# Optimization experiments

Hardware: AMD Instinct MI355X
Metric: run time of the kernel (lower is better)

Reference implementation:

```python
import jax, jax.numpy as jnp
import numpy as np

N_NODES = 100000
N_EDGES = 3200000
D_IN = 256
D_HID = 256
D_OUT = 64


def setup_inputs() -> dict:
    key = jax.random.key(0)
    k1, k2, k3, k4 = jax.random.split(key, 4)
    x = jax.random.normal(k1, (N_NODES, D_IN), dtype=jnp.float32)
    edge_index = jax.random.randint(k2, (2, N_EDGES), 0, N_NODES, dtype=jnp.int32)
    W1 = jax.random.normal(k3, (D_IN, D_HID), dtype=jnp.float32) / np.sqrt(D_IN)
    b1 = jnp.zeros((D_HID,), dtype=jnp.float32)
    W2 = jax.random.normal(k4, (D_HID, D_OUT), dtype=jnp.float32) / np.sqrt(D_HID)
    b2 = jnp.zeros((D_OUT,), dtype=jnp.float32)
    return {"x": x, "edge_index": edge_index, "W1": W1, "b1": b1, "W2": W2, "b2": b2}


def _gcn_conv(x, src, dst, norm, W, b, n_nodes):
    # dense linear transform, then normalized scatter-add aggregation
    h = x @ W  # [N, out]
    msg = norm[:, None] * h[src]  # gather + scale, [E+N, out]
    out = jax.ops.segment_sum(msg, dst, num_segments=n_nodes)
    return out + b


def reference(x, edge_index, W1, b1, W2, b2):
    n = x.shape[0]
    # add self-loops (PyG GCNConv default)
    loops = jnp.arange(n, dtype=edge_index.dtype)
    src = jnp.concatenate([edge_index[0], loops])
    dst = jnp.concatenate([edge_index[1], loops])
    # symmetric normalization deg^{-1/2}[src] * deg^{-1/2}[dst]
    deg = jax.ops.segment_sum(jnp.ones_like(src, dtype=x.dtype), dst, num_segments=n)
    dinv = jnp.where(deg > 0, jax.lax.rsqrt(jnp.maximum(deg, 1.0)), 0.0)
    norm = dinv[src] * dinv[dst]

    h = _gcn_conv(x, src, dst, norm, W1, b1, n)
    h = jax.nn.relu(h)
    # dropout is identity at inference
    h = _gcn_conv(h, src, dst, norm, W2, b2, n)
    return jax.nn.log_softmax(h, axis=1)
```

## Files before the change

kernel.cpp:

```cpp
#include <hip/hip_runtime.h>
#include <hip/hip_bf16.h>


typedef __bf16 bf16;
typedef bf16 bf16x8 __attribute__((ext_vector_type(8)));
typedef float f32x4 __attribute__((ext_vector_type(4)));
typedef float f32x2 __attribute__((ext_vector_type(2)));

#define NBLK 256

__global__ __launch_bounds__(256) void k_b1(const int* __restrict__ edge, int E, int chunk,
                                            int NB, int* __restrict__ gcnt) {
    __shared__ int cnt[512];
    int tid = threadIdx.x;
    for (int i = tid; i < NB; i += 256) cnt[i] = 0;
    __syncthreads();
    int s = blockIdx.x * chunk, e = min(s + chunk, E);
    for (int i = s + tid; i < e; i += 256) atomicAdd(&cnt[edge[E + i] >> 9], 1);
    __syncthreads();
    for (int i = tid; i < NB; i += 256) gcnt[blockIdx.x * NB + i] = cnt[i];
}

__global__ void k_b2(const int* __restrict__ gcnt, int NB, int E, int* __restrict__ bstart) {
    __shared__ int col[256];
    int k = threadIdx.x;
    int sum = 0;
    if (k < NB)
        for (int b = 0; b < NBLK; ++b) sum += gcnt[b * NB + k];
    col[k] = sum;
    __syncthreads();
    for (int o = 1; o < 256; o <<= 1) {
        int v = (k >= o) ? col[k - o] : 0;
        __syncthreads();
        col[k] += v;
        __syncthreads();
    }
    if (k < NB) bstart[k] = col[k] - sum;
    if (k == 0) bstart[NB] = E;
}

__global__ void k_b2b(int* __restrict__ gcnt, int NB, const int* __restrict__ bstart) {
    __shared__ int col[256];
    int b = threadIdx.x;
    int k = blockIdx.x;
    int v = gcnt[b * NB + k];
    col[b] = v;
    __syncthreads();
    for (int o = 1; o < 256; o <<= 1) {
        int t = (b >= o) ? col[b - o] : 0;
        __syncthreads();
        col[b] += t;
        __syncthreads();
    }
    gcnt[b * NB + k] = bstart[k] + col[b] - v;
}

__global__ __launch_bounds__(256) void k_b3(const int* __restrict__ edge, int E, int chunk,
                                            int NB, const int* __restrict__ base,
                                            int* __restrict__ ebuf) {
    __shared__ int cnt[512];
    __shared__ int bs[512];
    int tid = threadIdx.x;
    for (int i = tid; i < NB; i += 256) {
        cnt[i] = 0;
        bs[i] = base[blockIdx.x * NB + i];
    }
    __syncthreads();
    int s = blockIdx.x * chunk, e = min(s + chunk, E);
    for (int i = s + tid; i < e; i += 256) {
        int sv = edge[i], dv = edge[E + i];
        int k = dv >> 9;
        int r = atomicAdd(&cnt[k], 1);
        ebuf[bs[k] + r] = sv | ((dv & 511) << 17);
    }
}

__global__ __launch_bounds__(256) void k_b45(const int* __restrict__ ebuf,
                                             const int* __restrict__ bstart,
                                             const float* __restrict__ scale, int n, int E,
                                             int NB, int* __restrict__ off,
                                             float* __restrict__ dinv,
                                             float* __restrict__ ws) {
    __shared__ int cnt[512];
    __shared__ int red[256];
    int tid = threadIdx.x;
    int k = blockIdx.x;
    cnt[tid] = 0;
    cnt[tid + 256] = 0;
    __syncthreads();
    int s = bstart[k], e = bstart[k + 1];
    for (int i = s + tid; i < e; i += 256) atomicAdd(&cnt[(ebuf[i] >> 17) & 511], 1);
    __syncthreads();
    int c0 = cnt[tid * 2], c1 = cnt[tid * 2 + 1];
    int sum = c0 + c1;
    red[tid] = sum;
    __syncthreads();
    for (int o = 1; o < 256; o <<= 1) {
        int v = (tid >= o) ? red[tid - o] : 0;
        __syncthreads();
        red[tid] += v;
        __syncthreads();
    }
    int ex = red[tid] - sum;
    int base = k << 9;
    int g0 = base + tid * 2, g1 = g0 + 1;
    int o0 = s + ex, o1 = s + ex + c0;
    if (g0 < n) {
        off[g0] = o0;
        float d0 = rsqrtf((float)(c0 + 1));
        dinv[g0] = d0;
        ws[g0] = d0 * scale[g0];
    } else if (g0 == n) off[g0] = o0;
    if (g1 < n) {
        off[g1] = o1;
        float d1 = rsqrtf((float)(c1 + 1));
        dinv[g1] = d1;
        ws[g1] = d1 * scale[g1];
    } else if (g1 == n) off[g1] = o1;
    if (k == NB - 1 && tid == 0) off[n] = E;
}

__global__ __launch_bounds__(256) void k_b6(const int* __restrict__ ebuf,
                                            const int* __restrict__ bstart,
                                            const int* __restrict__ off,
                                            const float* __restrict__ ws, int n,
                                            int2* __restrict__ pair) {
    __shared__ int cnt[512];
    __shared__ int offl[512];
    int tid = threadIdx.x;
    int k = blockIdx.x;
    int base = k << 9;
    cnt[tid] = 0;
    cnt[tid + 256] = 0;
    offl[tid] = (base + tid < n) ? off[base + tid] : 0;
    offl[tid + 256] = (base + 256 + tid < n) ? off[base + 256 + tid] : 0;
    __syncthreads();
    int s = bstart[k], e = bstart[k + 1];
    for (int i = s + tid; i < e; i += 256) {
        int pk = ebuf[i];
        int sv = pk & 0x1ffff;
        int node = (pk >> 17) & 511;
        int r = atomicAdd(&cnt[node], 1);
        pair[offl[node] + r] = make_int2(sv << 8, __float_as_int(ws[sv]));
    }
}

__global__ __launch_bounds__(256) void k_quant(const float* __restrict__ x,
                                               unsigned char* __restrict__ xq,
                                               float* __restrict__ scale, int n) {
    int row = blockIdx.x * 4 + (threadIdx.x >> 6);
    int lane = threadIdx.x & 63;
    if (row >= n) return;
    f32x4 v = ((const f32x4*)x)[(size_t)row * 64 + lane];
    float m = fmaxf(fmaxf(fabsf(v[0]), fabsf(v[1])), fmaxf(fabsf(v[2]), fabsf(v[3])));
    for (int o = 32; o > 0; o >>= 1) m = fmaxf(m, __shfl_xor(m, o));
    m = fmaxf(m, 1e-20f);
    float inv = 127.0f / m;
    int b0 = (__float2int_rn(v[0] * inv) + 128) & 255;
    int b1 = (__float2int_rn(v[1] * inv) + 128) & 255;
    int b2 = (__float2int_rn(v[2] * inv) + 128) & 255;
    int b3 = (__float2int_rn(v[3] * inv) + 128) & 255;
    ((int*)xq)[(size_t)row * 64 + lane] = b0 | (b1 << 8) | (b2 << 16) | (b3 << 24);
    if (lane == 0) scale[row] = m / 127.0f;
}

__global__ __launch_bounds__(256) void k_quant2(const bf16* __restrict__ tb,
                                                const float* __restrict__ dinv,
                                                unsigned char* __restrict__ tq,
                                                float* __restrict__ w2v, int n) {
    int t = blockIdx.x * 256 + threadIdx.x;
    int row = t >> 3;
    int l8 = t & 7;
    if (row >= n) return;
    bf16x8 v = ((const bf16x8*)tb)[(size_t)row * 8 + l8];
    float f[8], m = 0.0f;
#pragma unroll
    for (int j = 0; j < 8; ++j) { f[j] = (float)v[j]; m = fmaxf(m, fabsf(f[j])); }
    for (int o = 4; o > 0; o >>= 1) m = fmaxf(m, __shfl_xor(m, o));
    m = fmaxf(m, 1e-20f);
    float inv = 127.0f / m;
    int lo = 0, hi = 0;
#pragma unroll
    for (int j = 0; j < 4; ++j) lo |= ((__float2int_rn(f[j] * inv) + 128) & 255) << (8 * j);
#pragma unroll
    for (int j = 0; j < 4; ++j) hi |= ((__float2int_rn(f[4 + j] * inv) + 128) & 255) << (8 * j);
    ((int2*)tq)[(size_t)row * 8 + l8] = make_int2(lo, hi);
    if (l8 == 0) w2v[row] = dinv[row] * (m / 127.0f);
}

__global__ void k_wt(const float* __restrict__ W1, const float* __restrict__ W2,
                     bf16* __restrict__ W1t, bf16* __restrict__ W2t) {
    int b = blockIdx.x;
    int k = threadIdx.x;
    if (b < 256) W1t[b * 256 + k] = (bf16)W1[k * 256 + b];
    else { int nc = b - 256; W2t[nc * 256 + k] = (bf16)W2[k * 64 + nc]; }
}

__device__ __forceinline__ void acc16(f32x2 a[8], uint4 t, float w, float& wsum) {
    wsum += w;
    f32x2 w2 = {w, w};
    unsigned u0 = t.x, u1 = t.y, u2 = t.z, u3 = t.w;
    f32x2 c;
    c[0] = (float)(u0 & 255u);         c[1] = (float)((u0 >> 8) & 255u);  a[0] += w2 * c;
    c[0] = (float)((u0 >> 16) & 255u); c[1] = (float)(u0 >> 24);         a[1] += w2 * c;
    c[0] = (float)(u1 & 255u);         c[1] = (float)((u1 >> 8) & 255u);  a[2] += w2 * c;
    c[0] = (float)((u1 >> 16) & 255u); c[1] = (float)(u1 >> 24);         a[3] += w2 * c;
    c[0] = (float)(u2 & 255u);         c[1] = (float)((u2 >> 8) & 255u);  a[4] += w2 * c;
    c[0] = (float)((u2 >> 16) & 255u); c[1] = (float)(u2 >> 24);         a[5] += w2 * c;
    c[0] = (float)(u3 & 255u);         c[1] = (float)((u3 >> 8) & 255u);  a[6] += w2 * c;
    c[0] = (float)((u3 >> 16) & 255u); c[1] = (float)(u3 >> 24);         a[7] += w2 * c;
}

__device__ __forceinline__ void acc8(f32x2 a[4], int2 t, float w, float& wsum) {
    wsum += w;
    f32x2 w2 = {w, w};
    unsigned u0 = (unsigned)t.x, u1 = (unsigned)t.y;
    f32x2 c;
    c[0] = (float)(u0 & 255u);         c[1] = (float)((u0 >> 8) & 255u);  a[0] += w2 * c;
    c[0] = (float)((u0 >> 16) & 255u); c[1] = (float)(u0 >> 24);         a[1] += w2 * c;
    c[0] = (float)(u1 & 255u);         c[1] = (float)((u1 >> 8) & 255u);  a[2] += w2 * c;
    c[0] = (float)((u1 >> 16) & 255u); c[1] = (float)(u1 >> 24);         a[3] += w2 * c;
}

__global__ __launch_bounds__(256) void k_agg1(const unsigned char* __restrict__ xq,
                                              const float* __restrict__ wsv,
                                              const int* __restrict__ off,
                                              const int2* __restrict__ pair,
                                              const float* __restrict__ dinv,
                                              bf16* __restrict__ ax, int n) {
    int wv = blockIdx.x * 4 + (threadIdx.x >> 6);
    int lane = threadIdx.x & 63;
    int node = wv * 4 + (lane >> 4);
    int l16 = lane & 15;
    if (node >= n) return;
    int s0 = off[node], s1 = off[node + 1];
    float dv = dinv[node];
    const unsigned char* xqb = xq + l16 * 16;
    f32x2 a[8] = {};
    float wsum = 0.0f;
    uint4 xs = *(const uint4*)(xqb + (size_t)node * 256);
    acc16(a, xs, wsv[node], wsum);
    int e = s0;
    if (s1 - s0 >= 8) {
        int2 p[8];
#pragma unroll
        for (int q = 0; q < 8; ++q) p[q] = pair[s0 + q];
        e = s0 + 8;
        for (; e + 8 <= s1; e += 8) {
            uint4 t[8];
#pragma unroll
            for (int q = 0; q < 8; ++q)
                t[q] = *(const uint4*)(xqb + (unsigned)p[q].x);
            int2 pn[8];
#pragma unroll
            for (int q = 0; q < 8; ++q) pn[q] = pair[e + q];
#pragma unroll
            for (int q = 0; q < 8; ++q) acc16(a, t[q], __int_as_float(p[q].y), wsum);
#pragma unroll
            for (int q = 0; q < 8; ++q) p[q] = pn[q];
        }
        uint4 t[8];
#pragma unroll
        for (int q = 0; q < 8; ++q)
            t[q] = *(const uint4*)(xqb + (unsigned)p[q].x);
#pragma unroll
        for (int q = 0; q < 8; ++q) acc16(a, t[q], __int_as_float(p[q].y), wsum);
    }
    for (; e < s1; ++e) {
        int2 p = pair[e];
        uint4 t = *(const uint4*)(xqb + (unsigned)p.x);
        acc16(a, t, __int_as_float(p.y), wsum);
    }
    float c = 128.0f * wsum;
    bf16x8 o0, o1;
#pragma unroll
    for (int j = 0; j < 4; ++j) {
        o0[2 * j]     = (bf16)((a[j][0] - c) * dv);
        o0[2 * j + 1] = (bf16)((a[j][1] - c) * dv);
        o1[2 * j]     = (bf16)((a[4 + j][0] - c) * dv);
        o1[2 * j + 1] = (bf16)((a[4 + j][1] - c) * dv);
    }
    ((bf16x8*)ax)[(size_t)node * 32 + l16 * 2] = o0;
    ((bf16x8*)ax)[(size_t)node * 32 + l16 * 2 + 1] = o1;
}

__device__ __forceinline__ int swz(int s) { return s ^ ((s >> 3) & 7); }

__global__ __launch_bounds__(512) void k_gemmp(const bf16* __restrict__ A,
                                               const bf16* __restrict__ Bt,
                                               const float* __restrict__ bias,
                                               bf16* __restrict__ C, int n) {
    __shared__ __align__(16) bf16 As[8 * 64 * 8];
    __shared__ __align__(16) bf16 Bs[16 * 64 * 8];
    int tid = threadIdx.x;
    int bm = blockIdx.x * 128;
    int w = tid >> 6, lane = tid & 63;
    int wm = w >> 2;
    int wn = w & 3;

    int r = tid >> 2;
    int cq = tid & 3;
    int a_slot = swz(((r >> 4) * 64) + cq * 16 + (r & 15));
    int arow = bm + r; if (arow > n - 1) arow = n - 1;

    f32x4 acc[4][4] = {};

    for (int k0 = 0; k0 < 256; k0 += 32) {
        __syncthreads();
        uint4 av = *(const uint4*)(A + (size_t)arow * 256 + k0 + cq * 8);
        *(uint4*)(As + a_slot * 8) = av;
#pragma unroll
        for (int rep = 0; rep < 2; ++rep) {
            int r2 = rep * 128 + r;
            uint4 bv = *(const uint4*)(Bt + (size_t)r2 * 256 + k0 + cq * 8);
            *(uint4*)(Bs + swz(((r2 >> 4) * 64) + cq * 16 + (r2 & 15)) * 8) = bv;
        }
        __syncthreads();
        bf16x8 af[4], bfr[4];
#pragma unroll
        for (int i = 0; i < 4; ++i)
            af[i] = *(const bf16x8*)(As + swz(((wm * 4 + i) * 64) + lane) * 8);
#pragma unroll
        for (int j = 0; j < 4; ++j)
            bfr[j] = *(const bf16x8*)(Bs + swz(((wn * 4 + j) * 64) + lane) * 8);
#pragma unroll
        for (int i = 0; i < 4; ++i)
#pragma unroll
            for (int j = 0; j < 4; ++j)
                acc[i][j] = __builtin_amdgcn_mfma_f32_16x16x32_bf16(af[i], bfr[j], acc[i][j], 0, 0, 0);
    }

    int colb = lane & 15, rowq = lane >> 4;
#pragma unroll
    for (int i = 0; i < 4; ++i)
#pragma unroll
        for (int j = 0; j < 4; ++j) {
            int col = wn * 64 + j * 16 + colb;
            float bv = bias[col];
#pragma unroll
            for (int rr = 0; rr < 4; ++rr) {
                int row = bm + wm * 64 + i * 16 + rowq * 4 + rr;
                if (row < n) {
                    float v = acc[i][j][rr] + bv;
                    C[(size_t)row * 256 + col] = (bf16)(v > 0.0f ? v : 0.0f);
                }
            }
        }
}

__global__ __launch_bounds__(256) void k_gemm2(const bf16* __restrict__ A,
                                               const bf16* __restrict__ Bt,
                                               bf16* __restrict__ C, int n) {
    __shared__ __align__(16) bf16 As[4 * 64 * 8];
    __shared__ __align__(16) bf16 Bs[4 * 64 * 8];
    int tid = threadIdx.x;
    int bm = blockIdx.x * 64;
    int w = tid >> 6, lane = tid & 63;
    int wm = w >> 1, wn = w & 1;

    int r = tid >> 2;
    int cq = tid & 3;
    int lds_slot = swz(((r >> 4) * 64) + cq * 16 + (r & 15));
    int arow = bm + r; if (arow > n - 1) arow = n - 1;

    f32x4 acc[2][2] = {};

    for (int k0 = 0; k0 < 256; k0 += 32) {
        __syncthreads();
        uint4 av = *(const uint4*)(A + (size_t)arow * 256 + k0 + cq * 8);
        uint4 bv = *(const uint4*)(Bt + (size_t)r * 256 + k0 + cq * 8);
        *(uint4*)(As + lds_slot * 8) = av;
        *(uint4*)(Bs + lds_slot * 8) = bv;
        __syncthreads();
#pragma unroll
        for (int i = 0; i < 2; ++i) {
            bf16x8 af = *(const bf16x8*)(As + swz((wm * 2 + i) * 64 + lane) * 8);
#pragma unroll
            for (int j = 0; j < 2; ++j) {
                bf16x8 bfr = *(const bf16x8*)(Bs + swz((wn * 2 + j) * 64 + lane) * 8);
                acc[i][j] = __builtin_amdgcn_mfma_f32_16x16x32_bf16(af, bfr, acc[i][j], 0, 0, 0);
            }
        }
    }

    int colb = lane & 15, rowq = lane >> 4;
#pragma unroll
    for (int i = 0; i < 2; ++i) {
#pragma unroll
        for (int j = 0; j < 2; ++j) {
            int col = wn * 32 + j * 16 + colb;
#pragma unroll
            for (int rr = 0; rr < 4; ++rr) {
                int row = bm + wm * 32 + i * 16 + rowq * 4 + rr;
                if (row < n) C[(size_t)row * 64 + col] = (bf16)acc[i][j][rr];
            }
        }
    }
}

__global__ __launch_bounds__(256) void k_agg2(const unsigned char* __restrict__ tq,
                                              const float* __restrict__ w2v,
                                              const int* __restrict__ off,
                                              const int2* __restrict__ pair,
                                              const float* __restrict__ dinv,
                                              const float* __restrict__ b2,
                                              float* __restrict__ out, int n) {
    int wv = blockIdx.x * 4 + (threadIdx.x >> 6);
    int lane = threadIdx.x & 63;
    int node = wv * 8 + (lane >> 3);
    int l8 = lane & 7;
    if (node >= n) return;
    int s0 = off[node], s1 = off[node + 1];
    float dv = dinv[node];
    const unsigned char* tqb = tq + l8 * 8;
    int2 ts = *(const int2*)(tqb + (size_t)node * 64);
    f32x2 a[4] = {};
    float wsum = 0.0f;
    acc8(a, ts, w2v[node], wsum);
    int e = s0;
    if (s1 - s0 >= 8) {
        int2 p[8]; float sc[8];
#pragma unroll
        for (int q = 0; q < 8; ++q) p[q] = pair[s0 + q];
#pragma unroll
        for (int q = 0; q < 8; ++q) sc[q] = w2v[(unsigned)p[q].x >> 8];
        e = s0 + 8;
        for (; e + 8 <= s1; e += 8) {
            int2 t[8];
#pragma unroll
            for (int q = 0; q < 8; ++q) t[q] = *(const int2*)(tqb + ((unsigned)p[q].x >> 2));
            int2 pn[8];
#pragma unroll
            for (int q = 0; q < 8; ++q) pn[q] = pair[e + q];
            float scn[8];
#pragma unroll
            for (int q = 0; q < 8; ++q) scn[q] = w2v[(unsigned)pn[q].x >> 8];
#pragma unroll
            for (int q = 0; q < 8; ++q) acc8(a, t[q], sc[q], wsum);
#pragma unroll
            for (int q = 0; q < 8; ++q) { p[q] = pn[q]; sc[q] = scn[q]; }
        }
        int2 t[8];
#pragma unroll
        for (int q = 0; q < 8; ++q) t[q] = *(const int2*)(tqb + ((unsigned)p[q].x >> 2));
#pragma unroll
        for (int q = 0; q < 8; ++q) acc8(a, t[q], sc[q], wsum);
    }
    for (; e < s1; ++e) {
        int2 p = pair[e];
        float w = w2v[(unsigned)p.x >> 8];
        int2 t = *(const int2*)(tqb + ((unsigned)p.x >> 2));
        acc8(a, t, w, wsum);
    }
    float c = 128.0f * wsum;
    float aa[8];
#pragma unroll
    for (int j = 0; j < 4; ++j) { aa[2 * j] = a[j][0]; aa[2 * j + 1] = a[j][1]; }
    const float4* B2 = (const float4*)b2;
    float4 bv0 = B2[l8 * 2], bv1 = B2[l8 * 2 + 1];
    aa[0] = (aa[0] - c) * dv + bv0.x; aa[1] = (aa[1] - c) * dv + bv0.y;
    aa[2] = (aa[2] - c) * dv + bv0.z; aa[3] = (aa[3] - c) * dv + bv0.w;
    aa[4] = (aa[4] - c) * dv + bv1.x; aa[5] = (aa[5] - c) * dv + bv1.y;
    aa[6] = (aa[6] - c) * dv + bv1.z; aa[7] = (aa[7] - c) * dv + bv1.w;
    float m = aa[0];
#pragma unroll
    for (int j = 1; j < 8; ++j) m = fmaxf(m, aa[j]);
    for (int o = 4; o > 0; o >>= 1) m = fmaxf(m, __shfl_xor(m, o));
    float s = 0.0f;
#pragma unroll
    for (int j = 0; j < 8; ++j) s += __expf(aa[j] - m);
    for (int o = 4; o > 0; o >>= 1) s += __shfl_xor(s, o);
    float ls = m + __logf(s);
    f32x4 o0, o1;
    o0[0] = aa[0] - ls; o0[1] = aa[1] - ls; o0[2] = aa[2] - ls; o0[3] = aa[3] - ls;
    o1[0] = aa[4] - ls; o1[1] = aa[5] - ls; o1[2] = aa[6] - ls; o1[3] = aa[7] - ls;
    f32x4* O = (f32x4*)out;
    O[(size_t)node * 16 + l8 * 2] = o0;
    O[(size_t)node * 16 + l8 * 2 + 1] = o1;
}

extern "C" void kernel_launch(void* const* d_in, const int* in_sizes, int n_in,
                              void* d_out, int out_size, void* d_ws, size_t ws_size,
                              hipStream_t stream) {
    const float* x   = (const float*)d_in[0];
    const int*  edge = (const int*)d_in[1];
    const float* W1  = (const float*)d_in[2];
    const float* b1  = (const float*)d_in[3];
    const float* W2  = (const float*)d_in[4];
    const float* b2  = (const float*)d_in[5];
    float* out = (float*)d_out;

    int n = in_sizes[0] / 256;
    int E = in_sizes[1] / 2;
    int NB = (n + 511) >> 9;
    int chunk = (E + NBLK - 1) / NBLK;

    char* ws = (char*)d_ws;
    auto alloc = [&](size_t bytes) -> char* {
        char* p = ws;
        ws += (bytes + 255) & ~(size_t)255;
        return p;
    };
    int*   gcnt   = (int*)alloc((size_t)NBLK * NB * 4);
    int*   bstart = (int*)alloc((size_t)(NB + 1) * 4);
    int*   ebuf   = (int*)alloc((size_t)E * 4);
    float* dinv   = (float*)alloc((size_t)n * 4);
    float* wsv    = (float*)alloc((size_t)n * 4);
    int*   off    = (int*)alloc((size_t)(n + 1) * 4);
    int2*  pair   = (int2*)alloc((size_t)E * 8);
    unsigned char* xq = (unsigned char*)alloc((size_t)n * 256);
    float* scale  = (float*)alloc((size_t)n * 4);
    bf16*  ax     = (bf16*)alloc((size_t)n * 256 * 2);
    bf16*  h1     = (bf16*)alloc((size_t)n * 256 * 2);
    bf16*  tb     = (bf16*)alloc((size_t)n * 64 * 2);
    unsigned char* tq = (unsigned char*)alloc((size_t)n * 64);
    float* w2v    = (float*)alloc((size_t)n * 4);
    bf16*  W1t    = (bf16*)alloc(256 * 256 * 2);
    bf16*  W2t    = (bf16*)alloc(64 * 256 * 2);

    k_quant<<<(n + 3) / 4, 256, 0, stream>>>(x, xq, scale, n);

    k_b1<<<NBLK, 256, 0, stream>>>(edge, E, chunk, NB, gcnt);
    k_b2<<<1, 256, 0, stream>>>(gcnt, NB, E, bstart);
    k_b2b<<<NB, 256, 0, stream>>>(gcnt, NB, bstart);
    k_b3<<<NBLK, 256, 0, stream>>>(edge, E, chunk, NB, gcnt, ebuf);
    k_b45<<<NB, 256, 0, stream>>>(ebuf, bstart, scale, n, E, NB, off, dinv, wsv);
    k_b6<<<NB, 256, 0, stream>>>(ebuf, bstart, off, wsv, n, pair);

    k_wt<<<320, 256, 0, stream>>>(W1, W2, W1t, W2t);

    k_agg1<<<(n + 15) / 16, 256, 0, stream>>>(xq, wsv, off, pair, dinv, ax, n);
    k_gemmp<<<(n + 127) / 128, 512, 0, stream>>>(ax, W1t, b1, h1, n);

    k_gemm2<<<(n + 63) / 64, 256, 0, stream>>>(h1, W2t, tb, n);
    k_quant2<<<(n * 8 + 255) / 256, 256, 0, stream>>>(tb, dinv, tq, w2v, n);
    k_agg2<<<(n + 31) / 32, 256, 0, stream>>>(tq, w2v, off, pair, dinv, b2, out, n);
}
```

Before: 521.1 us.

## Split layer-1 aggregation into feature halves and fuse quantization into gemm2

The int8 feature table is stored as two 128-byte half tables, and the layer-1 aggregation runs in two passes, one per half. Each pass gathers from a 12.8 MB table instead of a 25.6 MB one, so the gathered rows are more likely to stay in cache, at the cost of reading the edge lists twice. Separately, the second GEMM now quantizes its output tile through shared memory and writes int8 rows plus scales directly. This removes the bf16 intermediate buffer and the separate quant2 launch.

```diff
diff --git a/kernel.cpp b/kernel.cpp
--- a/kernel.cpp
+++ b/kernel.cpp
@@ -146,7 +146,8 @@
 }
 
 __global__ __launch_bounds__(256) void k_quant(const float* __restrict__ x,
-                                               unsigned char* __restrict__ xq,
+                                               unsigned char* __restrict__ xqA,
+                                               unsigned char* __restrict__ xqB,
                                                float* __restrict__ scale, int n) {
     int row = blockIdx.x * 4 + (threadIdx.x >> 6);
     int lane = threadIdx.x & 63;
@@ -160,32 +161,10 @@
     int b1 = (__float2int_rn(v[1] * inv) + 128) & 255;
     int b2 = (__float2int_rn(v[2] * inv) + 128) & 255;
     int b3 = (__float2int_rn(v[3] * inv) + 128) & 255;
-    ((int*)xq)[(size_t)row * 64 + lane] = b0 | (b1 << 8) | (b2 << 16) | (b3 << 24);
+    int word = b0 | (b1 << 8) | (b2 << 16) | (b3 << 24);
+    if (lane < 32) ((int*)xqA)[(size_t)row * 32 + lane] = word;
+    else           ((int*)xqB)[(size_t)row * 32 + (lane - 32)] = word;
     if (lane == 0) scale[row] = m / 127.0f;
-}
-
-__global__ __launch_bounds__(256) void k_quant2(const bf16* __restrict__ tb,
-                                                const float* __restrict__ dinv,
-                                                unsigned char* __restrict__ tq,
-                                                float* __restrict__ w2v, int n) {
-    int t = blockIdx.x * 256 + threadIdx.x;
-    int row = t >> 3;
-    int l8 = t & 7;
-    if (row >= n) return;
-    bf16x8 v = ((const bf16x8*)tb)[(size_t)row * 8 + l8];
-    float f[8], m = 0.0f;
-#pragma unroll
-    for (int j = 0; j < 8; ++j) { f[j] = (float)v[j]; m = fmaxf(m, fabsf(f[j])); }
-    for (int o = 4; o > 0; o >>= 1) m = fmaxf(m, __shfl_xor(m, o));
-    m = fmaxf(m, 1e-20f);
-    float inv = 127.0f / m;
-    int lo = 0, hi = 0;
-#pragma unroll
-    for (int j = 0; j < 4; ++j) lo |= ((__float2int_rn(f[j] * inv) + 128) & 255) << (8 * j);
-#pragma unroll
-    for (int j = 0; j < 4; ++j) hi |= ((__float2int_rn(f[4 + j] * inv) + 128) & 255) << (8 * j);
-    ((int2*)tq)[(size_t)row * 8 + l8] = make_int2(lo, hi);
-    if (l8 == 0) w2v[row] = dinv[row] * (m / 127.0f);
 }
 
 __global__ void k_wt(const float* __restrict__ W1, const float* __restrict__ W2,
@@ -222,23 +201,23 @@
     c[0] = (float)((u1 >> 16) & 255u); c[1] = (float)(u1 >> 24);         a[3] += w2 * c;
 }
 
-__global__ __launch_bounds__(256) void k_agg1(const unsigned char* __restrict__ xq,
-                                              const float* __restrict__ wsv,
-                                              const int* __restrict__ off,
-                                              const int2* __restrict__ pair,
-                                              const float* __restrict__ dinv,
-                                              bf16* __restrict__ ax, int n) {
+__global__ __launch_bounds__(256) void k_agg1h(const unsigned char* __restrict__ xqh,
+                                               const float* __restrict__ wsv,
+                                               const int* __restrict__ off,
+                                               const int2* __restrict__ pair,
+                                               const float* __restrict__ dinv,
+                                               bf16* __restrict__ ax, int hofs, int n) {
     int wv = blockIdx.x * 4 + (threadIdx.x >> 6);
     int lane = threadIdx.x & 63;
-    int node = wv * 4 + (lane >> 4);
-    int l16 = lane & 15;
+    int node = wv * 8 + (lane >> 3);
+    int l8 = lane & 7;
     if (node >= n) return;
     int s0 = off[node], s1 = off[node + 1];
     float dv = dinv[node];
-    const unsigned char* xqb = xq + l16 * 16;
+    const unsigned char* xqb = xqh + l8 * 16;
     f32x2 a[8] = {};
     float wsum = 0.0f;
-    uint4 xs = *(const uint4*)(xqb + (size_t)node * 256);
+    uint4 xs = *(const uint4*)(xqb + (size_t)node * 128);
     acc16(a, xs, wsv[node], wsum);
     int e = s0;
     if (s1 - s0 >= 8) {
@@ -250,7 +229,7 @@
             uint4 t[8];
 #pragma unroll
             for (int q = 0; q < 8; ++q)
-                t[q] = *(const uint4*)(xqb + (unsigned)p[q].x);
+                t[q] = *(const uint4*)(xqb + ((unsigned)p[q].x >> 1));
             int2 pn[8];
 #pragma unroll
             for (int q = 0; q < 8; ++q) pn[q] = pair[e + q];
@@ -262,13 +241,13 @@
         uint4 t[8];
 #pragma unroll
         for (int q = 0; q < 8; ++q)
-            t[q] = *(const uint4*)(xqb + (unsigned)p[q].x);
+            t[q] = *(const uint4*)(xqb + ((unsigned)p[q].x >> 1));
 #pragma unroll
         for (int q = 0; q < 8; ++q) acc16(a, t[q], __int_as_float(p[q].y), wsum);
     }
     for (; e < s1; ++e) {
         int2 p = pair[e];
-        uint4 t = *(const uint4*)(xqb + (unsigned)p.x);
+        uint4 t = *(const uint4*)(xqb + ((unsigned)p.x >> 1));
         acc16(a, t, __int_as_float(p.y), wsum);
     }
     float c = 128.0f * wsum;
@@ -280,8 +259,8 @@
         o1[2 * j]     = (bf16)((a[4 + j][0] - c) * dv);
         o1[2 * j + 1] = (bf16)((a[4 + j][1] - c) * dv);
     }
-    ((bf16x8*)ax)[(size_t)node * 32 + l16 * 2] = o0;
-    ((bf16x8*)ax)[(size_t)node * 32 + l16 * 2 + 1] = o1;
+    ((bf16x8*)ax)[(size_t)node * 32 + hofs + l8 * 2] = o0;
+    ((bf16x8*)ax)[(size_t)node * 32 + hofs + l8 * 2 + 1] = o1;
 }
 
 __device__ __forceinline__ int swz(int s) { return s ^ ((s >> 3) & 7); }
@@ -348,11 +327,14 @@
         }
 }
 
-__global__ __launch_bounds__(256) void k_gemm2(const bf16* __restrict__ A,
-                                               const bf16* __restrict__ Bt,
-                                               bf16* __restrict__ C, int n) {
+__global__ __launch_bounds__(256) void k_gemm2q(const bf16* __restrict__ A,
+                                                const bf16* __restrict__ Bt,
+                                                const float* __restrict__ dinv,
+                                                unsigned char* __restrict__ tq,
+                                                float* __restrict__ w2v, int n) {
     __shared__ __align__(16) bf16 As[4 * 64 * 8];
     __shared__ __align__(16) bf16 Bs[4 * 64 * 8];
+    __shared__ float tbf[64][65];
     int tid = threadIdx.x;
     int bm = blockIdx.x * 64;
     int w = tid >> 6, lane = tid & 63;
@@ -384,17 +366,37 @@
     }
 
     int colb = lane & 15, rowq = lane >> 4;
-#pragma unroll
-    for (int i = 0; i < 2; ++i) {
-#pragma unroll
-        for (int j = 0; j < 2; ++j) {
-            int col = wn * 32 + j * 16 + colb;
-#pragma unroll
-            for (int rr = 0; rr < 4; ++rr) {
-                int row = bm + wm * 32 + i * 16 + rowq * 4 + rr;
-                if (row < n) C[(size_t)row * 64 + col] = (bf16)acc[i][j][rr];
-            }
+    __syncthreads();
+#pragma unroll
+    for (int i = 0; i < 2; ++i)
+#pragma unroll
+        for (int j = 0; j < 2; ++j)
+#pragma unroll
+            for (int rr = 0; rr < 4; ++rr)
+                tbf[wm * 32 + i * 16 + rowq * 4 + rr][wn * 32 + j * 16 + colb] = acc[i][j][rr];
+    __syncthreads();
+
+    int row = tid >> 2, l4 = tid & 3;
+    int grow = bm + row;
+    if (grow < n) {
+        float f[16], m = 0.0f;
+#pragma unroll
+        for (int k = 0; k < 16; ++k) { f[k] = tbf[row][l4 * 16 + k]; m = fmaxf(m, fabsf(f[k])); }
+        m = fmaxf(m, __shfl_xor(m, 1));
+        m = fmaxf(m, __shfl_xor(m, 2));
+        m = fmaxf(m, 1e-20f);
+        float inv = 127.0f / m;
+        int wd[4];
+#pragma unroll
+        for (int g = 0; g < 4; ++g) {
+            int acc_w = 0;
+#pragma unroll
+            for (int b = 0; b < 4; ++b)
+                acc_w |= ((__float2int_rn(f[g * 4 + b] * inv) + 128) & 255) << (8 * b);
+            wd[g] = acc_w;
         }
+        ((int4*)tq)[(size_t)grow * 4 + l4] = make_int4(wd[0], wd[1], wd[2], wd[3]);
+        if (l4 == 0) w2v[grow] = dinv[grow] * (m / 127.0f);
     }
 }
 
@@ -508,17 +510,17 @@
     float* wsv    = (float*)alloc((size_t)n * 4);
     int*   off    = (int*)alloc((size_t)(n + 1) * 4);
     int2*  pair   = (int2*)alloc((size_t)E * 8);
-    unsigned char* xq = (unsigned char*)alloc((size_t)n * 256);
+    unsigned char* xqA = (unsigned char*)alloc((size_t)n * 128);
+    unsigned char* xqB = (unsigned char*)alloc((size_t)n * 128);
     float* scale  = (float*)alloc((size_t)n * 4);
     bf16*  ax     = (bf16*)alloc((size_t)n * 256 * 2);
     bf16*  h1     = (bf16*)alloc((size_t)n * 256 * 2);
-    bf16*  tb     = (bf16*)alloc((size_t)n * 64 * 2);
     unsigned char* tq = (unsigned char*)alloc((size_t)n * 64);
     float* w2v    = (float*)alloc((size_t)n * 4);
     bf16*  W1t    = (bf16*)alloc(256 * 256 * 2);
     bf16*  W2t    = (bf16*)alloc(64 * 256 * 2);
 
-    k_quant<<<(n + 3) / 4, 256, 0, stream>>>(x, xq, scale, n);
+    k_quant<<<(n + 3) / 4, 256, 0, stream>>>(x, xqA, xqB, scale, n);
 
     k_b1<<<NBLK, 256, 0, stream>>>(edge, E, chunk, NB, gcnt);
     k_b2<<<1, 256, 0, stream>>>(gcnt, NB, E, bstart);
@@ -529,10 +531,10 @@
 
     k_wt<<<320, 256, 0, stream>>>(W1, W2, W1t, W2t);
 
-    k_agg1<<<(n + 15) / 16, 256, 0, stream>>>(xq, wsv, off, pair, dinv, ax, n);
+    k_agg1h<<<(n + 31) / 32, 256, 0, stream>>>(xqA, wsv, off, pair, dinv, ax, 0, n);
+    k_agg1h<<<(n + 31) / 32, 256, 0, stream>>>(xqB, wsv, off, pair, dinv, ax, 16, n);
     k_gemmp<<<(n + 127) / 128, 512, 0, stream>>>(ax, W1t, b1, h1, n);
 
-    k_gemm2<<<(n + 63) / 64, 256, 0, stream>>>(h1, W2t, tb, n);
-    k_quant2<<<(n * 8 + 255) / 256, 256, 0, stream>>>(tb, dinv, tq, w2v, n);
+    k_gemm2q<<<(n + 63) / 64, 256, 0, stream>>>(h1, W2t, dinv, tq, w2v, n);
     k_agg2<<<(n + 31) / 32, 256, 0, stream>>>(tq, w2v, off, pair, dinv, b2, out, n);
 }
```

Result: no change. 526.2 us (+1.0%).
